# Kernel optimization log

Hardware: AMD Instinct MI355X
Metric: run time of the kernel (lower is better)

The kernel has to match this reference:

```python
import jax, jax.numpy as jnp
import numpy as np

EPS = 1e-5

def mesh_conv(x, gemm, w, b):
    # x: [B, C, E] edge features; gemm: [B, E, 4] int neighbor edge ids
    B, C, E = x.shape
    self_idx = jnp.broadcast_to(jnp.arange(E, dtype=gemm.dtype)[None, :, None], (B, E, 1))
    G = jnp.concatenate([self_idx, gemm], axis=2) + 1          # [B, E, 5], 0 = zero-pad slot
    xp = jnp.concatenate([jnp.zeros((B, C, 1), x.dtype), x], axis=2)  # [B, C, E+1]
    # f[b,c,e,k] = xp[b,c,G[b,e,k]]
    f = jax.vmap(lambda xb, gb: xb[:, gb])(xp, G)              # [B, C, E, 5]
    f0 = f[..., 0]
    x1 = f[..., 1] + f[..., 3]
    x2 = f[..., 2] + f[..., 4]
    x3 = jnp.abs(f[..., 1] - f[..., 3])
    x4 = jnp.abs(f[..., 2] - f[..., 4])
    Gm = jnp.stack([f0, x1, x2, x3, x4], axis=-1)              # [B, C, E, 5]
    # Conv2d kernel (1,5) over the 5 symmetric features
    out = jnp.einsum('bces,ocs->boe', Gm, w) + b[None, :, None]
    return out

def instance_norm(x):
    # InstanceNorm2d (affine=False): normalize per (b, c) over edge dim
    mean = jnp.mean(x, axis=2, keepdims=True)
    var = jnp.var(x, axis=2, keepdims=True)
    return (x - mean) * jax.lax.rsqrt(var + EPS)

def setup_inputs() -> dict:
    key = jax.random.key(0)
    ks = jax.random.split(key, 6)
    B, Cin, Cout, E = 2, 64, 128, 100000
    fe = jax.random.normal(ks[0], (B, Cin, E), dtype=jnp.float32)
    gemm = jax.random.randint(ks[1], (B, E, 4), 0, E, dtype=jnp.int32)
    w1 = jax.random.normal(ks[2], (Cout, Cin, 5), dtype=jnp.float32) * 0.05
    b1 = jax.random.normal(ks[3], (Cout,), dtype=jnp.float32) * 0.05
    w2 = jax.random.normal(ks[4], (Cout, Cout, 5), dtype=jnp.float32) * 0.05
    b2 = jax.random.normal(ks[5], (Cout,), dtype=jnp.float32) * 0.05
    return {"fe": fe, "gemm": gemm, "w1": w1, "b1": b1, "w2": w2, "b2": b2}

def reference(fe, gemm, w1, b1, w2, b2):
    x1 = jax.nn.relu(instance_norm(mesh_conv(fe, gemm, w1, b1)))
    x2 = instance_norm(mesh_conv(x1, gemm, w2, b2))
    x2 = jax.nn.relu(x2 + x1)
    return x2  # [B, Cout, E]; pool=0 so before_pool is None
```

## Files before the change

### kernel.cpp

```cpp
#include <hip/hip_runtime.h>

typedef unsigned short u16;
typedef __attribute__((ext_vector_type(4))) unsigned short u16x4;
typedef __attribute__((ext_vector_type(8))) unsigned short u16x8;
typedef __attribute__((ext_vector_type(8))) short s16x8;
typedef __attribute__((ext_vector_type(4))) float f32x4;

__device__ __forceinline__ float bf2f(u16 u){
  union { unsigned int i; float f; } v; v.i = ((unsigned int)u) << 16; return v.f;
}
__device__ __forceinline__ u16 f2bf(float f){
  union { float f; unsigned int i; } v; v.f = f;
  unsigned int r = v.i + 0x7fffu + ((v.i >> 16) & 1u);
  return (u16)(r >> 16);
}

__global__ __launch_bounds__(256) void prep_w(
    const float* __restrict__ src, u16* __restrict__ dst, int cout, int cin)
{
  const int n = cout * cin * 5;
  const int i = blockIdx.x * 256 + threadIdx.x;
  if (i >= n) return;
  const int o   = i / (cin * 5);
  const int rem = i - o * cin * 5;
  const int s   = rem / cin;
  const int c   = rem - s * cin;
  dst[i] = f2bf(src[(o * cin + c) * 5 + s]);
}

__global__ __launch_bounds__(256) void transpose64(
    const float* __restrict__ x, u16* __restrict__ xT, int E)
{
  __shared__ u16 tile[64][66];
  const int b   = blockIdx.z;
  const int e0  = blockIdx.x * 64;
  const int col = threadIdx.x & 63;
  const int r   = threadIdx.x >> 6;
  const int e   = e0 + col;
  #pragma unroll
  for (int k = 0; k < 16; k++) {
    const int c = r * 16 + k;
    float v = 0.f;
    if (e < E) v = x[((size_t)b * 64 + c) * (size_t)E + e];
    tile[c][col] = f2bf(v);
  }
  __syncthreads();
  const int e_l  = threadIdx.x >> 2;
  const int part = threadIdx.x & 3;
  const int eg   = e0 + e_l;
  if (eg < E) {
    u16* dst = xT + ((size_t)b * E + eg) * 64 + part * 16;
    #pragma unroll
    for (int h = 0; h < 2; h++) {
      u16x8 v;
      #pragma unroll
      for (int cc = 0; cc < 8; cc++) v[cc] = tile[part * 16 + h * 8 + cc][e_l];
      *(u16x8*)(dst + h * 8) = v;
    }
  }
}

__global__ __launch_bounds__(512, 8) void conv1_mfma(
    const u16* __restrict__ xT, const int* __restrict__ gidx,
    const u16* __restrict__ W, const float* __restrict__ bias,
    u16* __restrict__ y1b, float2* __restrict__ partials, int E, int nbx)
{
  constexpr int CIN = 64, EPB = 64, SUB = 8;
  constexpr int KK  = CIN * 5;
  constexpr int NT  = EPB / 16;
  __shared__ __align__(16) u16 F[5 * EPB * CIN];

  const int b  = blockIdx.z;
  const int bx = blockIdx.x;
  const int t  = threadIdx.x;
  const int e_l = t / SUB;
  const int sub = t % SUB;
  const size_t e_raw = (size_t)bx * EPB + e_l;
  const int e = (int)(e_raw < (size_t)E ? e_raw : (size_t)(E - 1));

  int rows[5];
  {
    const int4 g = *(const int4*)(gidx + ((size_t)b * E + e) * 4);
    rows[0] = e; rows[1] = g.x; rows[2] = g.y; rows[3] = g.z; rows[4] = g.w;
  }
  const u16* base = xT + (size_t)b * E * CIN + sub * 8;

  u16x8 raw[5];
  #pragma unroll
  for (int j = 0; j < 5; j++)
    raw[j] = *(const u16x8*)(base + (size_t)rows[j] * CIN);
  __builtin_amdgcn_sched_barrier(0);

  {
    const int pc = (sub ^ (e_l & 7)) * 8;
    u16x8 o1, o2, o3, o4;
    #pragma unroll
    for (int c = 0; c < 8; c++) {
      const float a1 = bf2f(raw[1][c]), a2 = bf2f(raw[2][c]);
      const float a3 = bf2f(raw[3][c]), a4 = bf2f(raw[4][c]);
      o1[c] = f2bf(a1 + a3);
      o2[c] = f2bf(a2 + a4);
      o3[c] = f2bf(fabsf(a1 - a3));
      o4[c] = f2bf(fabsf(a2 - a4));
    }
    *(u16x8*)&F[(0 * EPB + e_l) * CIN + pc] = raw[0];
    *(u16x8*)&F[(1 * EPB + e_l) * CIN + pc] = o1;
    *(u16x8*)&F[(2 * EPB + e_l) * CIN + pc] = o2;
    *(u16x8*)&F[(3 * EPB + e_l) * CIN + pc] = o3;
    *(u16x8*)&F[(4 * EPB + e_l) * CIN + pc] = o4;
  }
  __syncthreads();

  const int lane = t & 63, wv = t >> 6;
  const int lr = lane & 15, quad = lane >> 4;
  f32x4 acc[NT];
  #pragma unroll
  for (int j = 0; j < NT; j++) acc[j] = (f32x4){0.f, 0.f, 0.f, 0.f};
  #pragma unroll
  for (int kt = 0; kt < KK / 32; kt++) {
    const int s   = (kt * 32) / CIN;
    const int cb  = (kt * 32) % CIN;
    const int ko  = kt * 32 + quad * 8;
    const int chk = ((cb >> 3) + quad) ^ (lr & 7);
    const s16x8 a0 = *(const s16x8*)(W + (size_t)(wv * 16 + lr) * KK + ko);
    #pragma unroll
    for (int j = 0; j < NT; j++) {
      const s16x8 bj = *(const s16x8*)&F[(s * EPB + j * 16 + lr) * CIN + chk * 8];
      acc[j] = __builtin_amdgcn_mfma_f32_16x16x32_bf16(bj, a0, acc[j], 0, 0, 0);
    }
  }

  const int ch = wv * 16 + lr;
  const float bv = bias[ch];
  float s = 0.f, s2 = 0.f;
  #pragma unroll
  for (int j = 0; j < NT; j++) {
    #pragma unroll
    for (int r = 0; r < 4; r++) {
      const int el = j * 16 + quad * 4 + r;
      const size_t eg = (size_t)bx * EPB + el;
      if (eg < (size_t)E) {
        const float v = acc[j][r] + bv;
        y1b[((size_t)b * E + eg) * 128 + ch] = f2bf(v);
        s += v; s2 += v * v;
      }
    }
  }
  s  += __shfl_xor(s, 16);  s  += __shfl_xor(s, 32);
  s2 += __shfl_xor(s2, 16); s2 += __shfl_xor(s2, 32);
  if (lane < 16)
    partials[(size_t)(b * 128 + ch) * nbx + bx] = make_float2(s, s2);
}

__global__ __launch_bounds__(512, 8) void conv2_mfma(
    const u16* __restrict__ x1b, const int* __restrict__ gidx,
    const u16* __restrict__ W, const float* __restrict__ bias,
    const float2* __restrict__ stats1,
    float* __restrict__ y2, float2* __restrict__ partials, int E, int nbx)
{
  constexpr int CIN = 128, EPB = 32, SUB = 16;
  constexpr int KK  = CIN * 5;
  constexpr int NT  = EPB / 16;
  __shared__ __align__(16) u16 F[5 * EPB * CIN];

  const int b  = blockIdx.z;
  const int bx = blockIdx.x;
  const int t  = threadIdx.x;
  const int e_l = t / SUB;
  const int sub = t % SUB;
  const size_t e_raw = (size_t)bx * EPB + e_l;
  const int e = (int)(e_raw < (size_t)E ? e_raw : (size_t)(E - 1));

  int rows[5];
  {
    const int4 g = *(const int4*)(gidx + ((size_t)b * E + e) * 4);
    rows[0] = e; rows[1] = g.x; rows[2] = g.y; rows[3] = g.z; rows[4] = g.w;
  }
  const u16* base = x1b + (size_t)b * E * 128 + sub * 8;

  u16x8 raw[5];
  #pragma unroll
  for (int j = 0; j < 5; j++)
    raw[j] = *(const u16x8*)(base + (size_t)rows[j] * 128);
  f32x4 st[4];
  {
    const float* sp = (const float*)(stats1 + b * 128 + sub * 8);
    #pragma unroll
    for (int q = 0; q < 4; q++) st[q] = *(const f32x4*)(sp + q * 4);
  }
  __builtin_amdgcn_sched_barrier(0);

  {
    const int pc = (sub ^ (e_l & 7)) * 8;
    u16x8 o0, o1, o2, o3, o4;
    #pragma unroll
    for (int c = 0; c < 8; c++) {
      const float m = st[c >> 1][(c & 1) * 2];
      const float r = st[c >> 1][(c & 1) * 2 + 1];
      float x[5];
      #pragma unroll
      for (int j = 0; j < 5; j++) {
        float v = (bf2f(raw[j][c]) - m) * r;
        x[j] = v < 0.f ? 0.f : v;
      }
      o0[c] = f2bf(x[0]);
      o1[c] = f2bf(x[1] + x[3]);
      o2[c] = f2bf(x[2] + x[4]);
      o3[c] = f2bf(fabsf(x[1] - x[3]));
      o4[c] = f2bf(fabsf(x[2] - x[4]));
    }
    *(u16x8*)&F[(0 * EPB + e_l) * CIN + pc] = o0;
    *(u16x8*)&F[(1 * EPB + e_l) * CIN + pc] = o1;
    *(u16x8*)&F[(2 * EPB + e_l) * CIN + pc] = o2;
    *(u16x8*)&F[(3 * EPB + e_l) * CIN + pc] = o3;
    *(u16x8*)&F[(4 * EPB + e_l) * CIN + pc] = o4;
  }
  __syncthreads();

  const int lane = t & 63, wv = t >> 6;
  const int lr = lane & 15, quad = lane >> 4;
  f32x4 acc[NT];
  #pragma unroll
  for (int j = 0; j < NT; j++) acc[j] = (f32x4){0.f, 0.f, 0.f, 0.f};
  #pragma unroll
  for (int kt = 0; kt < KK / 32; kt++) {
    const int s   = (kt * 32) / CIN;
    const int cb  = (kt * 32) % CIN;
    const int ko  = kt * 32 + quad * 8;
    const int chk = ((cb >> 3) + quad) ^ (lr & 7);
    const s16x8 a0 = *(const s16x8*)(W + (size_t)(wv * 16 + lr) * KK + ko);
    #pragma unroll
    for (int j = 0; j < NT; j++) {
      const s16x8 bj = *(const s16x8*)&F[(s * EPB + j * 16 + lr) * CIN + chk * 8];
      acc[j] = __builtin_amdgcn_mfma_f32_16x16x32_bf16(a0, bj, acc[j], 0, 0, 0);
    }
  }

  const size_t ybase = (size_t)b * 128;
  const int m0 = wv * 16 + quad * 4;
  const float4 bs = *(const float4*)(bias + m0);
  #pragma unroll
  for (int r = 0; r < 4; r++) {
    const int m = m0 + r;
    const float bv = ((const float*)&bs)[r];
    float s = 0.f, s2 = 0.f;
    #pragma unroll
    for (int j = 0; j < NT; j++) {
      const size_t eg = (size_t)bx * EPB + j * 16 + lr;
      if (eg < (size_t)E) {
        const float v = acc[j][r] + bv;
        y2[(ybase + m) * E + eg] = v;
        s += v; s2 += v * v;
      }
    }
    #pragma unroll
    for (int mk = 1; mk < 16; mk <<= 1) {
      s  += __shfl_xor(s,  mk);
      s2 += __shfl_xor(s2, mk);
    }
    if (lr == 0)
      partials[(size_t)(b * 128 + m) * nbx + bx] = make_float2(s, s2);
  }
}

__global__ __launch_bounds__(256) void stats_finalize(
    const float2* __restrict__ partials, float2* __restrict__ stats,
    int nbx, int E)
{
  const int row = blockIdx.x;
  const float2* p = partials + (size_t)row * nbx;
  float s = 0.f, s2 = 0.f;
  for (int i = threadIdx.x; i < nbx; i += 256) {
    const float2 v = p[i];
    s += v.x; s2 += v.y;
  }
  #pragma unroll
  for (int off = 32; off > 0; off >>= 1) {
    s  += __shfl_down(s, off);
    s2 += __shfl_down(s2, off);
  }
  __shared__ float rs[4], rs2[4];
  const int wv = threadIdx.x >> 6;
  if ((threadIdx.x & 63) == 0) { rs[wv] = s; rs2[wv] = s2; }
  __syncthreads();
  if (threadIdx.x == 0) {
    s  = rs[0] + rs[1] + rs[2] + rs[3];
    s2 = rs2[0] + rs2[1] + rs2[2] + rs2[3];
    const float mean = s / E;
    const float var  = s2 / E - mean * mean;
    stats[row] = make_float2(mean, rsqrtf(var + 1e-5f));
  }
}

__global__ __launch_bounds__(256) void final_k(
    const float* __restrict__ y2, const u16* __restrict__ y1b,
    const float2* __restrict__ st1, const float2* __restrict__ st2,
    float* __restrict__ out, int E)
{
  __shared__ float tile[32][65];
  const int b  = blockIdx.z;
  const int o0 = blockIdx.y * 32;
  const int e0 = blockIdx.x * 64;
  const int t  = threadIdx.x;

  {
    const int e_l  = t >> 2;
    const int part = t & 3;
    const int eg   = e0 + e_l;
    if (eg < E) {
      const u16* src = y1b + ((size_t)b * E + eg) * 128 + o0 + part * 8;
      const u16x8 v = *(const u16x8*)src;
      #pragma unroll
      for (int i = 0; i < 8; i++) {
        const float2 s1 = st1[b * 128 + o0 + part * 8 + i];
        float x = (bf2f(v[i]) - s1.x) * s1.y;
        tile[part * 8 + i][e_l] = x < 0.f ? 0.f : x;
      }
    }
  }
  __syncthreads();

  {
    const int col = t & 63;
    const int r   = t >> 6;
    const int eg  = e0 + col;
    if (eg < E) {
      #pragma unroll
      for (int k = 0; k < 8; k++) {
        const int o = o0 + r * 8 + k;
        const float2 s2 = st2[b * 128 + o];
        const size_t idx = ((size_t)b * 128 + o) * E + eg;
        float v = (y2[idx] - s2.x) * s2.y + tile[r * 8 + k][col];
        v = v < 0.f ? 0.f : v;
        __builtin_nontemporal_store(v, out + idx);
      }
    }
  }
}

extern "C" void kernel_launch(void* const* d_in, const int* in_sizes, int n_in,
                              void* d_out, int out_size, void* d_ws, size_t ws_size,
                              hipStream_t stream)
{
  const float* fe  = (const float*)d_in[0];
  const int*   gmm = (const int*)d_in[1];
  const float* w1  = (const float*)d_in[2];
  const float* b1  = (const float*)d_in[3];
  const float* w2  = (const float*)d_in[4];
  const float* b2  = (const float*)d_in[5];
  float* out = (float*)d_out;

  const int B = 2, CIN = 64, COUT = 128;
  const int E = in_sizes[0] / (B * CIN);
  const int nbx1 = (E + 63) / 64;
  const int nbx2 = (E + 31) / 32;

  char* p = (char*)d_ws;
  auto alloc = [&](size_t bytes) -> char* {
    char* q = p; p += (bytes + 255) & ~(size_t)255; return q;
  };
  const size_t feT_b = (size_t)B * E * CIN * 2;
  const size_t y2_b  = (size_t)B * COUT * E * 4;
  char* regA = alloc(y2_b > feT_b ? y2_b : feT_b);
  u16*   feT = (u16*)regA;
  float* y2  = (float*)regA;
  u16*   y1b = (u16*)alloc((size_t)B * E * COUT * 2);
  float2* stats1 = (float2*)alloc((size_t)B * COUT * sizeof(float2));
  float2* stats2 = (float2*)alloc((size_t)B * COUT * sizeof(float2));
  u16* w1b = (u16*)alloc((size_t)COUT * CIN * 5 * 2);
  u16* w2b = (u16*)alloc((size_t)COUT * COUT * 5 * 2);
  float2* partials = (float2*)d_out;

  const int n_w1 = COUT * CIN * 5, n_w2 = COUT * COUT * 5;
  prep_w <<<dim3((n_w1 + 255) / 256), 256, 0, stream>>>(w1, w1b, COUT, CIN);
  prep_w <<<dim3((n_w2 + 255) / 256), 256, 0, stream>>>(w2, w2b, COUT, COUT);

  transpose64 <<<dim3((E + 63) / 64, 1, B), 256, 0, stream>>>(fe, feT, E);
  conv1_mfma <<<dim3(nbx1, 1, B), 512, 0, stream>>>(feT, gmm, w1b, b1, y1b, partials, E, nbx1);
  stats_finalize <<<dim3(B * COUT), 256, 0, stream>>>(partials, stats1, nbx1, E);
  conv2_mfma <<<dim3(nbx2, 1, B), 512, 0, stream>>>(y1b, gmm, w2b, b2, stats1, y2, partials, E, nbx2);
  stats_finalize <<<dim3(B * COUT), 256, 0, stream>>>(partials, stats2, nbx2, E);
  final_k <<<dim3((E + 63) / 64, COUT / 32, B), 256, 0, stream>>>(y2, y1b, stats1, stats2, out, E);
}
```

Baseline: 404.4 us.

## Pre-pack MFMA weight fragments and fold norm stats into FMA form

The weight-prep kernel now writes bf16 weights in the exact per-wave, per-lane MFMA fragment order, so each lane loads its A operand from a contiguous, coalesced address (wbase + kt*512) instead of a strided row gather. Instance-norm stats are stored as (-mean*rstd, rstd), so normalization becomes a single FMA in conv2 and the final kernel. The launch-bounds occupancy hint is lowered from 8 to 6, which gives the compiler more registers per thread but may reduce resident waves.

```diff
diff --git a/kernel.cpp b/kernel.cpp
--- a/kernel.cpp
+++ b/kernel.cpp
@@ -18,13 +18,18 @@
 __global__ __launch_bounds__(256) void prep_w(
     const float* __restrict__ src, u16* __restrict__ dst, int cout, int cin)
 {
-  const int n = cout * cin * 5;
+  const int n  = cout * cin * 5;
+  const int KT = (cin * 5) / 32;
   const int i = blockIdx.x * 256 + threadIdx.x;
   if (i >= n) return;
-  const int o   = i / (cin * 5);
-  const int rem = i - o * cin * 5;
-  const int s   = rem / cin;
-  const int c   = rem - s * cin;
+  const int ii   = i & 7;
+  const int lane = (i >> 3) & 63;
+  const int kt   = (i >> 9) % KT;
+  const int wv   = i / (KT * 512);
+  const int o = wv * 16 + (lane & 15);
+  const int k = kt * 32 + (lane >> 4) * 8 + ii;
+  const int s = k / cin;
+  const int c = k - s * cin;
   dst[i] = f2bf(src[(o * cin + c) * 5 + s]);
 }
 
@@ -60,13 +65,12 @@
   }
 }
 
-__global__ __launch_bounds__(512, 8) void conv1_mfma(
+__global__ __launch_bounds__(512, 6) void conv1_mfma(
     const u16* __restrict__ xT, const int* __restrict__ gidx,
-    const u16* __restrict__ W, const float* __restrict__ bias,
+    const u16* __restrict__ Wp, const float* __restrict__ bias,
     u16* __restrict__ y1b, float2* __restrict__ partials, int E, int nbx)
 {
-  constexpr int CIN = 64, EPB = 64, SUB = 8;
-  constexpr int KK  = CIN * 5;
+  constexpr int CIN = 64, EPB = 64, SUB = 8, KT = 10;
   constexpr int NT  = EPB / 16;
   __shared__ __align__(16) u16 F[5 * EPB * CIN];
 
@@ -75,6 +79,8 @@
   const int t  = threadIdx.x;
   const int e_l = t / SUB;
   const int sub = t % SUB;
+  const int lane = t & 63, wv = t >> 6;
+  const int lr = lane & 15, quad = lane >> 4;
   const size_t e_raw = (size_t)bx * EPB + e_l;
   const int e = (int)(e_raw < (size_t)E ? e_raw : (size_t)(E - 1));
 
@@ -84,6 +90,7 @@
     rows[0] = e; rows[1] = g.x; rows[2] = g.y; rows[3] = g.z; rows[4] = g.w;
   }
   const u16* base = xT + (size_t)b * E * CIN + sub * 8;
+  const u16* wbase = Wp + ((size_t)wv * KT * 64 + lane) * 8;
 
   u16x8 raw[5];
   #pragma unroll
@@ -111,18 +118,14 @@
   }
   __syncthreads();
 
-  const int lane = t & 63, wv = t >> 6;
-  const int lr = lane & 15, quad = lane >> 4;
   f32x4 acc[NT];
   #pragma unroll
   for (int j = 0; j < NT; j++) acc[j] = (f32x4){0.f, 0.f, 0.f, 0.f};
   #pragma unroll
-  for (int kt = 0; kt < KK / 32; kt++) {
-    const int s   = (kt * 32) / CIN;
-    const int cb  = (kt * 32) % CIN;
-    const int ko  = kt * 32 + quad * 8;
+  for (int kt = 0; kt < KT; kt++) {
+    const int s  = kt >> 1, cb = (kt & 1) * 32;
     const int chk = ((cb >> 3) + quad) ^ (lr & 7);
-    const s16x8 a0 = *(const s16x8*)(W + (size_t)(wv * 16 + lr) * KK + ko);
+    const s16x8 a0 = *(const s16x8*)(wbase + kt * 512);
     #pragma unroll
     for (int j = 0; j < NT; j++) {
       const s16x8 bj = *(const s16x8*)&F[(s * EPB + j * 16 + lr) * CIN + chk * 8];
@@ -152,14 +155,13 @@
     partials[(size_t)(b * 128 + ch) * nbx + bx] = make_float2(s, s2);
 }
 
-__global__ __launch_bounds__(512, 8) void conv2_mfma(
+__global__ __launch_bounds__(512, 6) void conv2_mfma(
     const u16* __restrict__ x1b, const int* __restrict__ gidx,
-    const u16* __restrict__ W, const float* __restrict__ bias,
+    const u16* __restrict__ Wp, const float* __restrict__ bias,
     const float2* __restrict__ stats1,
     float* __restrict__ y2, float2* __restrict__ partials, int E, int nbx)
 {
-  constexpr int CIN = 128, EPB = 32, SUB = 16;
-  constexpr int KK  = CIN * 5;
+  constexpr int CIN = 128, EPB = 32, SUB = 16, KT = 20;
   constexpr int NT  = EPB / 16;
   __shared__ __align__(16) u16 F[5 * EPB * CIN];
 
@@ -168,6 +170,8 @@
   const int t  = threadIdx.x;
   const int e_l = t / SUB;
   const int sub = t % SUB;
+  const int lane = t & 63, wv = t >> 6;
+  const int lr = lane & 15, quad = lane >> 4;
   const size_t e_raw = (size_t)bx * EPB + e_l;
   const int e = (int)(e_raw < (size_t)E ? e_raw : (size_t)(E - 1));
 
@@ -177,6 +181,7 @@
     rows[0] = e; rows[1] = g.x; rows[2] = g.y; rows[3] = g.z; rows[4] = g.w;
   }
   const u16* base = x1b + (size_t)b * E * 128 + sub * 8;
+  const u16* wbase = Wp + ((size_t)wv * KT * 64 + lane) * 8;
 
   u16x8 raw[5];
   #pragma unroll
@@ -195,12 +200,12 @@
     u16x8 o0, o1, o2, o3, o4;
     #pragma unroll
     for (int c = 0; c < 8; c++) {
-      const float m = st[c >> 1][(c & 1) * 2];
-      const float r = st[c >> 1][(c & 1) * 2 + 1];
+      const float nm = st[c >> 1][(c & 1) * 2];
+      const float rr = st[c >> 1][(c & 1) * 2 + 1];
       float x[5];
       #pragma unroll
       for (int j = 0; j < 5; j++) {
-        float v = (bf2f(raw[j][c]) - m) * r;
+        float v = fmaf(bf2f(raw[j][c]), rr, nm);
         x[j] = v < 0.f ? 0.f : v;
       }
       o0[c] = f2bf(x[0]);
@@ -217,18 +222,14 @@
   }
   __syncthreads();
 
-  const int lane = t & 63, wv = t >> 6;
-  const int lr = lane & 15, quad = lane >> 4;
   f32x4 acc[NT];
   #pragma unroll
   for (int j = 0; j < NT; j++) acc[j] = (f32x4){0.f, 0.f, 0.f, 0.f};
   #pragma unroll
-  for (int kt = 0; kt < KK / 32; kt++) {
-    const int s   = (kt * 32) / CIN;
-    const int cb  = (kt * 32) % CIN;
-    const int ko  = kt * 32 + quad * 8;
+  for (int kt = 0; kt < KT; kt++) {
+    const int s  = kt >> 2, cb = (kt & 3) * 32;
     const int chk = ((cb >> 3) + quad) ^ (lr & 7);
-    const s16x8 a0 = *(const s16x8*)(W + (size_t)(wv * 16 + lr) * KK + ko);
+    const s16x8 a0 = *(const s16x8*)(wbase + kt * 512);
     #pragma unroll
     for (int j = 0; j < NT; j++) {
       const s16x8 bj = *(const s16x8*)&F[(s * EPB + j * 16 + lr) * CIN + chk * 8];
@@ -288,7 +289,8 @@
     s2 = rs2[0] + rs2[1] + rs2[2] + rs2[3];
     const float mean = s / E;
     const float var  = s2 / E - mean * mean;
-    stats[row] = make_float2(mean, rsqrtf(var + 1e-5f));
+    const float rstd = rsqrtf(var + 1e-5f);
+    stats[row] = make_float2(-mean * rstd, rstd);
   }
 }
 
@@ -313,7 +315,7 @@
       #pragma unroll
       for (int i = 0; i < 8; i++) {
         const float2 s1 = st1[b * 128 + o0 + part * 8 + i];
-        float x = (bf2f(v[i]) - s1.x) * s1.y;
+        float x = fmaf(bf2f(v[i]), s1.y, s1.x);
         tile[part * 8 + i][e_l] = x < 0.f ? 0.f : x;
       }
     }
@@ -330,7 +332,7 @@
         const int o = o0 + r * 8 + k;
         const float2 s2 = st2[b * 128 + o];
         const size_t idx = ((size_t)b * 128 + o) * E + eg;
-        float v = (y2[idx] - s2.x) * s2.y + tile[r * 8 + k][col];
+        float v = fmaf(y2[idx], s2.y, s2.x) + tile[r * 8 + k][col];
         v = v < 0.f ? 0.f : v;
         __builtin_nontemporal_store(v, out + idx);
       }
```

After: 335.7 us. 17.0% less time.
